# Kernel tuning notes

Measured on AMD Instinct MI355X. Metric: run time of the kernel, lower is better.

The kernel has to match this reference:

```python
import jax, jax.numpy as jnp
import numpy as np

B, S, D, H, DK, DV = 4, 2048, 1024, 16, 64, 64

def setup_inputs() -> dict:
    key = jax.random.key(0)
    ks = jax.random.split(key, 7)
    scale = 0.02
    queries = jax.random.normal(ks[0], (B, S, D), jnp.float32)
    keys_ = jax.random.normal(ks[1], (B, S, D), jnp.float32)
    values = jax.random.normal(ks[2], (B, S, D), jnp.float32)
    # causal mask: 1 where attendable, 0 where masked
    mask = jnp.tril(jnp.ones((S, S), jnp.int32))[None, None, :, :]
    W_Q = jax.random.normal(ks[3], (D, H * DK), jnp.float32) * scale
    W_K = jax.random.normal(ks[4], (D, H * DK), jnp.float32) * scale
    W_V = jax.random.normal(ks[5], (D, H * DV), jnp.float32) * scale
    W_O = jax.random.normal(ks[6], (H * DV, D), jnp.float32) * scale
    return {"queries": queries, "keys": keys_, "values": values, "mask": mask,
            "W_Q": W_Q, "W_K": W_K, "W_V": W_V, "W_O": W_O}

def reference(queries, keys, values, mask, W_Q, W_K, W_V, W_O):
    b, skv, _ = keys.shape
    sq = queries.shape[1]
    scaling = 1.0 / (DK ** 0.5)
    Q = (queries @ W_Q).reshape(b, sq, H, DK)   # [B,Sq,H,DK]
    K = (keys @ W_K).reshape(b, skv, H, DK)     # [B,Skv,H,DK]
    V = (values @ W_V).reshape(b, skv, H, DV)   # [B,Skv,H,DV]
    scores = jnp.einsum('bqhd,bkhd->bhqk', Q, K)
    scores = jnp.where(mask == 0, -jnp.inf, scores)
    probs = jax.nn.softmax(scores * scaling, axis=-1)
    attn = jnp.einsum('bhqk,bkhd->bqhd', probs, V).reshape(b, sq, H * DV)
    return attn @ W_O
```

## Files before the change

### kernel.cpp

```cpp
#include <hip/hip_runtime.h>
#include <hip/hip_bf16.h>


typedef __attribute__((ext_vector_type(8))) __bf16 bf16x8;
typedef __attribute__((ext_vector_type(8))) unsigned short ushort8v;
typedef __attribute__((ext_vector_type(4))) unsigned short ushort4v;
typedef __attribute__((ext_vector_type(4))) unsigned uint4v;
typedef __attribute__((ext_vector_type(2))) unsigned uint2v;
typedef __attribute__((ext_vector_type(4))) float float4v;

#define MFMA16(a, b, c) __builtin_amdgcn_mfma_f32_16x16x32_bf16((a), (b), (c), 0, 0, 0)
#define GLDS16(g, l)                                                     \
    __builtin_amdgcn_global_load_lds(                                    \
        (const __attribute__((address_space(1))) void*)(g),              \
        (__attribute__((address_space(3))) void*)(l), 16, 0, 0)

__device__ __forceinline__ unsigned short f2bf(float f) {
    union { float f; unsigned u; } v; v.f = f;
    unsigned r = v.u + 0x7fffu + ((v.u >> 16) & 1u);
    return (unsigned short)(r >> 16);
}
__device__ __forceinline__ unsigned pkbf(float a, float b) {
    union { float f; unsigned u; } x, y; x.f = a; y.f = b;
    return __builtin_amdgcn_perm(y.u + 0x8000u, x.u + 0x8000u, 0x07060302u);
}
__device__ __forceinline__ float exp2_fast(float x) {
#if __has_builtin(__builtin_amdgcn_exp2f)
    return __builtin_amdgcn_exp2f(x);
#else
    return __builtin_exp2f(x);
#endif
}

__global__ __launch_bounds__(256) void transpose_w4(
    const float* __restrict__ W0, const float* __restrict__ W1,
    const float* __restrict__ W2, const float* __restrict__ W3,
    unsigned short* __restrict__ T0, unsigned short* __restrict__ T1,
    unsigned short* __restrict__ T2, unsigned short* __restrict__ T3)
{
    __shared__ unsigned short T[64][72];
    const int z = blockIdx.z;
    const float* W = z == 0 ? W0 : z == 1 ? W1 : z == 2 ? W2 : W3;
    unsigned short* Wt = z == 0 ? T0 : z == 1 ? T1 : z == 2 ? T2 : T3;
    const float scale = (z == 1) ? 0.125f * 1.44269504088896f : 1.0f;
    const int t = threadIdx.x;
    const int n0 = blockIdx.x * 64, k0 = blockIdx.y * 64;
    for (int i = 0; i < 4; i++) {
        int idx = i * 256 + t, r = idx >> 4, c = (idx & 15) * 4;
        float4v v = *(const float4v*)&W[(size_t)(k0 + r) * 1024 + n0 + c];
        T[c + 0][r] = f2bf(v.x * scale); T[c + 1][r] = f2bf(v.y * scale);
        T[c + 2][r] = f2bf(v.z * scale); T[c + 3][r] = f2bf(v.w * scale);
    }
    __syncthreads();
    for (int i = 0; i < 4; i++) {
        int idx = i * 256 + t, r = idx >> 4, c = (idx & 15) * 4;
        ushort4v o; o.x = T[r][c]; o.y = T[r][c + 1]; o.z = T[r][c + 2]; o.w = T[r][c + 3];
        *(ushort4v*)&Wt[(size_t)(n0 + r) * 1024 + k0 + c] = o;
    }
}

__global__ __launch_bounds__(256) void qkv_gemm(
    const float* __restrict__ Aq, const float* __restrict__ Ak,
    const float* __restrict__ Av,
    const unsigned short* __restrict__ WQt, const unsigned short* __restrict__ WKt,
    const unsigned short* __restrict__ WVt,
    unsigned short* __restrict__ Qb, unsigned short* __restrict__ Kb,
    unsigned short* __restrict__ Vto)
{
    __shared__ __align__(16) unsigned short As[128 * 64];
    __shared__ __align__(16) unsigned short Bs[128 * 64];

    const int t = threadIdx.x;
    const int lane = t & 63, w = t >> 6;
    const int lanelo = lane & 15, quad = lane >> 4;
    const int wm = w >> 1, wn = w & 1;
    const int rsw = (lanelo & 7) << 3;

    const int d = blockIdx.x;
    const int xcd = d & 7;
    const int s = d >> 3;
    const int group = s >> 6;
    const int u = s & 63;
    const bool vsw = (group == 2);

    const float* act; const unsigned short* wt; unsigned short* out;
    if (group == 0)      { act = Aq; wt = WQt; out = Qb; }
    else if (group == 1) { act = Ak; wt = WKt; out = Kb; }
    else                 { act = Av; wt = WVt; out = Vto; }

    const int big = (((u >> 3) << 3) | xcd) * 128;
    const int sml = (u & 7) * 128;
    int m0, n0, ldc;
    if (!vsw) { m0 = big; n0 = sml; ldc = 1024; }
    else      { n0 = big; m0 = sml; ldc = 8192; }
    const int act0 = vsw ? n0 : m0;
    const int wt0  = vsw ? m0 : n0;
    unsigned short* actS = vsw ? Bs : As;
    unsigned short* wtS  = vsw ? As : Bs;

    float4v acc[4][4];
    for (int i = 0; i < 4; i++)
        for (int j = 0; j < 4; j++) acc[i][j] = (float4v)(0.f);

    for (int k0 = 0; k0 < 1024; k0 += 64) {
        for (int i = 0; i < 4; i++) {
            int idx = i * 256 + t, row = idx >> 3, ch = idx & 7;
            GLDS16(wt + (size_t)(wt0 + row) * 1024 + k0 + ((ch ^ (row & 7)) << 3),
                   &wtS[idx * 8]);
        }
        for (int i = 0; i < 4; i++) {
            int si = i * 256 + t, row = si >> 3, ch = si & 7;
            const float* ap = act + (size_t)(act0 + row) * 1024 + k0 + ch * 8;
            float4v x = *(const float4v*)ap;
            float4v y = *(const float4v*)(ap + 4);
            uint4v o4 = { pkbf(x.x, x.y), pkbf(x.z, x.w),
                          pkbf(y.x, y.y), pkbf(y.z, y.w) };
            *(uint4v*)&actS[row * 64 + ((ch ^ (row & 7)) << 3)] = o4;
        }
        __syncthreads();
        for (int ks = 0; ks < 2; ks++) {
            bf16x8 af[4], bfr[4];
            for (int mi = 0; mi < 4; mi++)
                af[mi] = *(const bf16x8*)
                    &As[(wm * 64 + mi * 16 + lanelo) * 64 + ((ks * 32 + quad * 8) ^ rsw)];
            for (int ni = 0; ni < 4; ni++)
                bfr[ni] = *(const bf16x8*)
                    &Bs[(wn * 64 + ni * 16 + lanelo) * 64 + ((ks * 32 + quad * 8) ^ rsw)];
            for (int mi = 0; mi < 4; mi++)
                for (int ni = 0; ni < 4; ni++)
                    acc[mi][ni] = MFMA16(af[mi], bfr[ni], acc[mi][ni]);
        }
        __syncthreads();
    }

    for (int mi = 0; mi < 4; mi++)
        for (int ni = 0; ni < 4; ni++) {
            int col = n0 + wn * 64 + ni * 16 + lanelo;
            for (int rr = 0; rr < 4; rr++) {
                int row = m0 + wm * 64 + mi * 16 + quad * 4 + rr;
                out[(size_t)row * ldc + col] = f2bf(acc[mi][ni][rr]);
            }
        }
}

__global__ __launch_bounds__(256) void gemm_bb(
    const unsigned short* __restrict__ A, const unsigned short* __restrict__ Bt,
    float* __restrict__ Cp, int M, int N, int K)
{
    __shared__ __align__(16) unsigned short As[128 * 64];
    __shared__ __align__(16) unsigned short Bs[128 * 64];

    const int t = threadIdx.x;
    const int lane = t & 63, w = t >> 6;
    const int lanelo = lane & 15, quad = lane >> 4;
    const int wm = w >> 1, wn = w & 1;
    const int rsw = (lanelo & 7) << 3;

    const int d = blockIdx.x;
    const int xcd = d & 7, s = d >> 3;
    const int m0 = ((((s >> 3) << 3) | xcd)) * 128;
    const int n0 = (s & 7) * 128;

    float4v acc[4][4];
    for (int i = 0; i < 4; i++)
        for (int j = 0; j < 4; j++) acc[i][j] = (float4v)(0.f);

    for (int k0 = 0; k0 < K; k0 += 64) {
        for (int i = 0; i < 4; i++) {
            int idx = i * 256 + t, row = idx >> 3, ch = idx & 7;
            GLDS16(A + (size_t)(m0 + row) * K + k0 + ((ch ^ (row & 7)) << 3),
                   &As[idx * 8]);
        }
        for (int i = 0; i < 4; i++) {
            int idx = i * 256 + t, row = idx >> 3, ch = idx & 7;
            GLDS16(Bt + (size_t)(n0 + row) * K + k0 + ((ch ^ (row & 7)) << 3),
                   &Bs[idx * 8]);
        }
        __syncthreads();
        for (int ks = 0; ks < 2; ks++) {
            bf16x8 af[4], bfr[4];
            for (int mi = 0; mi < 4; mi++)
                af[mi] = *(const bf16x8*)
                    &As[(wm * 64 + mi * 16 + lanelo) * 64 + ((ks * 32 + quad * 8) ^ rsw)];
            for (int ni = 0; ni < 4; ni++)
                bfr[ni] = *(const bf16x8*)
                    &Bs[(wn * 64 + ni * 16 + lanelo) * 64 + ((ks * 32 + quad * 8) ^ rsw)];
            for (int mi = 0; mi < 4; mi++)
                for (int ni = 0; ni < 4; ni++)
                    acc[mi][ni] = MFMA16(af[mi], bfr[ni], acc[mi][ni]);
        }
        __syncthreads();
    }

    for (int mi = 0; mi < 4; mi++)
        for (int ni = 0; ni < 4; ni++) {
            int col = n0 + wn * 64 + ni * 16 + lanelo;
            for (int r = 0; r < 4; r++) {
                int row = m0 + wm * 64 + mi * 16 + quad * 4 + r;
                Cp[(size_t)row * N + col] = acc[mi][ni][r];
            }
        }
}

__global__ __launch_bounds__(256, 4) void attn_k(
    const unsigned short* __restrict__ Qb, const unsigned short* __restrict__ Kb,
    const unsigned short* __restrict__ Vt, unsigned short* __restrict__ Ob)
{
    __shared__ __align__(16) unsigned short Ks[2][64 * 64];
    __shared__ __align__(16) unsigned short Vs[2][64 * 64];
    __shared__ __align__(16) unsigned short Ps[4][16 * 64];

    const int t = threadIdx.x;
    const int lane = t & 63, w = t >> 6;
    const int lanelo = lane & 15, quad = lane >> 4;
    const int bh = blockIdx.x;
    const int b = bh >> 4, h = bh & 15;

    unsigned short* pw = &Ps[w][0];
    const int rsw = (lanelo & 7) * 8;
    const int l7 = lanelo & 7;

    auto stage = [&](int buf, int kt) {
        for (int i = 0; i < 2; i++) {
            int idx = i * 256 + t, row = idx >> 3, ch = idx & 7;
            GLDS16(Kb + ((size_t)(b * 2048 + kt * 64 + row)) * 1024 + h * 64
                       + ((ch ^ (row & 7)) << 3),
                   &Ks[buf][idx * 8]);
        }
        for (int i = 0; i < 2; i++) {
            int idx = i * 256 + t, row = idx >> 3, ch = idx & 7;
            GLDS16(Vt + (size_t)(h * 64 + row) * 8192 + b * 2048 + kt * 64
                       + ((ch ^ (row & 7)) << 3),
                   &Vs[buf][idx * 8]);
        }
    };

    for (int half = 0; half < 2; half++) {
        const int qt = half ? blockIdx.y : 31 - blockIdx.y;
        const int qb = qt * 64;
        const int nkt = qt + 1;
        const int q = qb + w * 16 + lanelo;

        bf16x8 qf[2];
        {
            const unsigned short* qp = Qb + ((size_t)(b * 2048) + q) * 1024 + h * 64 + quad * 8;
            qf[0] = *(const bf16x8*)(qp);
            qf[1] = *(const bf16x8*)(qp + 32);
        }
        float4v o[4];
        for (int i = 0; i < 4; i++) o[i] = (float4v)(0.f);
        float m_ = -__builtin_inff(), l_ = 0.f;

        stage(0, 0);
        __syncthreads();

        int cur = 0;
        for (int kt = 0; kt < nkt; kt++) {
            if (kt + 1 < nkt) stage(cur ^ 1, kt + 1);

            const unsigned short* ks = &Ks[cur][0];
            const unsigned short* vs = &Vs[cur][0];

            float4v sc[4];
            for (int nt = 0; nt < 4; nt++) {
                sc[nt] = (float4v)(0.f);
                for (int c = 0; c < 2; c++) {
                    bf16x8 kf = *(const bf16x8*)
                        &ks[(nt * 16 + lanelo) * 64 + ((c * 32 + quad * 8) ^ rsw)];
                    sc[nt] = MFMA16(kf, qf[c], sc[nt]);
                }
            }
            if (kt == nkt - 1) {
                const int kb0 = qb + quad * 4;
                for (int nt = 0; nt < 4; nt++)
                    for (int r = 0; r < 4; r++)
                        if (kb0 + nt * 16 + r > q) sc[nt][r] = -__builtin_inff();
            }
            float mx = sc[0][0];
            for (int nt = 0; nt < 4; nt++)
                for (int r = 0; r < 4; r++) mx = fmaxf(mx, sc[nt][r]);
            mx = fmaxf(mx, __shfl_xor(mx, 16, 64));
            mx = fmaxf(mx, __shfl_xor(mx, 32, 64));
            if (!__all(mx <= m_ + 8.f)) {
                float mnew = fmaxf(m_, mx);
                float alpha = exp2_fast(m_ - mnew);
                l_ *= alpha;
                for (int vt = 0; vt < 4; vt++)
                    for (int r = 0; r < 4; r++) o[vt][r] *= alpha;
                m_ = mnew;
            }
            float rs = 0.f;
            for (int nt = 0; nt < 4; nt++)
                for (int r = 0; r < 4; r++) {
                    float e = exp2_fast(sc[nt][r] - m_);
                    sc[nt][r] = e; rs += e;
                }
            rs += __shfl_xor(rs, 16, 64);
            rs += __shfl_xor(rs, 32, 64);
            l_ += rs;

            for (int nt = 0; nt < 4; nt++) {
                uint2v pv;
                pv.x = pkbf(sc[nt][0], sc[nt][1]);
                pv.y = pkbf(sc[nt][2], sc[nt][3]);
                *(uint2v*)((char*)pw + lanelo * 128
                           + ((((nt << 1) | (quad >> 1)) ^ l7) << 4)
                           + ((quad & 1) << 3)) = pv;
            }
            asm volatile("s_waitcnt lgkmcnt(0)" ::: "memory");
            __builtin_amdgcn_sched_barrier(0);
            for (int c = 0; c < 2; c++) {
                bf16x8 pf = *(const bf16x8*)((const char*)pw + lanelo * 128
                                             + (((c * 4 + quad) ^ l7) << 4));
                for (int vt = 0; vt < 4; vt++) {
                    bf16x8 vf = *(const bf16x8*)
                        &vs[(vt * 16 + lanelo) * 64 + ((c * 32 + quad * 8) ^ rsw)];
                    o[vt] = MFMA16(vf, pf, o[vt]);
                }
            }
            __syncthreads();
            cur ^= 1;
        }

        float inv = 1.0f / l_;
        for (int vt = 0; vt < 4; vt++) {
            uint2v ov;
            ov.x = pkbf(o[vt][0] * inv, o[vt][1] * inv);
            ov.y = pkbf(o[vt][2] * inv, o[vt][3] * inv);
            *(uint2v*)((char*)pw + lanelo * 128
                       + ((((vt << 1) | (quad >> 1)) ^ l7) << 4)
                       + ((quad & 1) << 3)) = ov;
        }
        asm volatile("s_waitcnt lgkmcnt(0)" ::: "memory");
        __builtin_amdgcn_sched_barrier(0);
        for (int i = 0; i < 2; i++) {
            int qr = i * 8 + (lane >> 3);
            int ch = lane & 7;
            ushort8v ov = *(const ushort8v*)((const char*)pw + qr * 128
                                             + ((ch ^ (qr & 7)) << 4));
            *(ushort8v*)(Ob + ((size_t)(b * 2048) + qb + w * 16 + qr) * 1024
                         + h * 64 + ch * 8) = ov;
        }
    }
}

extern "C" void kernel_launch(void* const* d_in, const int* in_sizes, int n_in,
                              void* d_out, int out_size, void* d_ws, size_t ws_size,
                              hipStream_t stream) {
    const float* queries = (const float*)d_in[0];
    const float* keys    = (const float*)d_in[1];
    const float* values  = (const float*)d_in[2];
    const float* W_Q = (const float*)d_in[4];
    const float* W_K = (const float*)d_in[5];
    const float* W_V = (const float*)d_in[6];
    const float* W_O = (const float*)d_in[7];

    const size_t SZ = (size_t)4 * 2048 * 1024;
    const size_t WSZ = (size_t)1024 * 1024;
    unsigned short* Qb  = (unsigned short*)d_ws;
    unsigned short* Kb  = Qb + SZ;
    unsigned short* Vt  = Kb + SZ;
    unsigned short* Ab  = Vt + SZ;
    unsigned short* WQt = Ab + SZ;
    unsigned short* WKt = WQt + WSZ;
    unsigned short* WVt = WKt + WSZ;
    unsigned short* WOt = WVt + WSZ;

    dim3 blk(256);
    hipLaunchKernelGGL(transpose_w4, dim3(16, 16, 4), blk, 0, stream,
                       W_Q, W_K, W_V, W_O, WQt, WKt, WVt, WOt);

    hipLaunchKernelGGL(qkv_gemm, dim3(1536), blk, 0, stream,
                       queries, keys, values, WQt, WKt, WVt, Qb, Kb, Vt);

    hipLaunchKernelGGL(attn_k, dim3(64, 16), blk, 0, stream, Qb, Kb, Vt, Ab);

    hipLaunchKernelGGL(gemm_bb, dim3(512), blk, 0, stream,
                       Ab, WOt, (float*)d_out, 8192, 1024, 1024);
}
```

Before: 314.9 us.

## Double-buffer gemm_bb LDS tiles and use partial vmcnt waits in attention

The output-projection GEMM now double-buffers its A/B LDS tiles, issuing the next k-tile's global-to-LDS loads before computing on the current one and waiting only for the older batch with a partial vmcnt. The attention kernel replaces its full __syncthreads with partial vmcnt waits plus raw barriers, so prefetch loads of the next K/V tile can stay in flight during compute. This aims to overlap memory latency with MFMA work. The cost is doubled LDS in the GEMM, which may reduce occupancy. Correctness now depends on hand-counted vmcnt values and the hardcoded 16-iteration loop, which assumes K=1024.

```diff
diff --git a/kernel.cpp b/kernel.cpp
--- a/kernel.cpp
+++ b/kernel.cpp
@@ -147,8 +147,8 @@
     const unsigned short* __restrict__ A, const unsigned short* __restrict__ Bt,
     float* __restrict__ Cp, int M, int N, int K)
 {
-    __shared__ __align__(16) unsigned short As[128 * 64];
-    __shared__ __align__(16) unsigned short Bs[128 * 64];
+    __shared__ __align__(16) unsigned short As[2][128 * 64];
+    __shared__ __align__(16) unsigned short Bs[2][128 * 64];
 
     const int t = threadIdx.x;
     const int lane = t & 63, w = t >> 6;
@@ -161,35 +161,48 @@
     const int m0 = ((((s >> 3) << 3) | xcd)) * 128;
     const int n0 = (s & 7) * 128;
 
+    auto stage = [&](int buf, int k0) {
+        for (int i = 0; i < 4; i++) {
+            int idx = i * 256 + t, row = idx >> 3, ch = idx & 7;
+            GLDS16(A + (size_t)(m0 + row) * K + k0 + ((ch ^ (row & 7)) << 3),
+                   &As[buf][idx * 8]);
+        }
+        for (int i = 0; i < 4; i++) {
+            int idx = i * 256 + t, row = idx >> 3, ch = idx & 7;
+            GLDS16(Bt + (size_t)(n0 + row) * K + k0 + ((ch ^ (row & 7)) << 3),
+                   &Bs[buf][idx * 8]);
+        }
+    };
+
     float4v acc[4][4];
     for (int i = 0; i < 4; i++)
         for (int j = 0; j < 4; j++) acc[i][j] = (float4v)(0.f);
 
-    for (int k0 = 0; k0 < K; k0 += 64) {
-        for (int i = 0; i < 4; i++) {
-            int idx = i * 256 + t, row = idx >> 3, ch = idx & 7;
-            GLDS16(A + (size_t)(m0 + row) * K + k0 + ((ch ^ (row & 7)) << 3),
-                   &As[idx * 8]);
-        }
-        for (int i = 0; i < 4; i++) {
-            int idx = i * 256 + t, row = idx >> 3, ch = idx & 7;
-            GLDS16(Bt + (size_t)(n0 + row) * K + k0 + ((ch ^ (row & 7)) << 3),
-                   &Bs[idx * 8]);
-        }
-        __syncthreads();
+    stage(0, 0);
+    for (int tt = 0; tt < 16; ++tt) {
+        const int cur = tt & 1;
+        if (tt + 1 < 16) {
+            stage(cur ^ 1, (tt + 1) * 64);
+            asm volatile("s_waitcnt vmcnt(8)" ::: "memory");
+        } else {
+            asm volatile("s_waitcnt vmcnt(0)" ::: "memory");
+        }
+        __builtin_amdgcn_s_barrier();
+        __builtin_amdgcn_sched_barrier(0);
         for (int ks = 0; ks < 2; ks++) {
             bf16x8 af[4], bfr[4];
             for (int mi = 0; mi < 4; mi++)
                 af[mi] = *(const bf16x8*)
-                    &As[(wm * 64 + mi * 16 + lanelo) * 64 + ((ks * 32 + quad * 8) ^ rsw)];
+                    &As[cur][(wm * 64 + mi * 16 + lanelo) * 64 + ((ks * 32 + quad * 8) ^ rsw)];
             for (int ni = 0; ni < 4; ni++)
                 bfr[ni] = *(const bf16x8*)
-                    &Bs[(wn * 64 + ni * 16 + lanelo) * 64 + ((ks * 32 + quad * 8) ^ rsw)];
+                    &Bs[cur][(wn * 64 + ni * 16 + lanelo) * 64 + ((ks * 32 + quad * 8) ^ rsw)];
             for (int mi = 0; mi < 4; mi++)
                 for (int ni = 0; ni < 4; ni++)
                     acc[mi][ni] = MFMA16(af[mi], bfr[ni], acc[mi][ni]);
         }
-        __syncthreads();
+        __builtin_amdgcn_sched_barrier(0);
+        __builtin_amdgcn_s_barrier();
     }
 
     for (int mi = 0; mi < 4; mi++)
@@ -252,11 +265,17 @@
         float m_ = -__builtin_inff(), l_ = 0.f;
 
         stage(0, 0);
-        __syncthreads();
 
         int cur = 0;
         for (int kt = 0; kt < nkt; kt++) {
-            if (kt + 1 < nkt) stage(cur ^ 1, kt + 1);
+            if (kt + 1 < nkt) {
+                stage(cur ^ 1, kt + 1);
+                asm volatile("s_waitcnt vmcnt(4)" ::: "memory");
+            } else {
+                asm volatile("s_waitcnt vmcnt(0)" ::: "memory");
+            }
+            __builtin_amdgcn_s_barrier();
+            __builtin_amdgcn_sched_barrier(0);
 
             const unsigned short* ks = &Ks[cur][0];
             const unsigned short* vs = &Vs[cur][0];
@@ -318,7 +337,8 @@
                     o[vt] = MFMA16(vf, pf, o[vt]);
                 }
             }
-            __syncthreads();
+            __builtin_amdgcn_sched_barrier(0);
+            __builtin_amdgcn_s_barrier();
             cur ^= 1;
         }
 
```

Result: no change. 312.7 us (median of 2 runs) (-0.7%).

## Split-K output GEMM with atomics and finer-grained waits in attention loop

Applied to the files above, without the earlier changes.

The output-projection GEMM is split in two along K, launching 1024 blocks instead of 512 for better occupancy. Partial results are accumulated into a zeroed output with float atomicAdd, which adds a memset and atomic traffic. Separately, the attention kernel replaces __syncthreads with explicit vmcnt waits and raw barriers, so the prefetch of the next K/V tile can stay in flight while the current tile is consumed. The correctness of vmcnt(4) relies on stage() issuing exactly four loads per thread, and the atomics make the summation order nondeterministic.

```diff
diff --git a/kernel.cpp b/kernel.cpp
--- a/kernel.cpp
+++ b/kernel.cpp
@@ -143,7 +143,7 @@
         }
 }
 
-__global__ __launch_bounds__(256) void gemm_bb(
+__global__ __launch_bounds__(256) void gemm_bb_sk(
     const unsigned short* __restrict__ A, const unsigned short* __restrict__ Bt,
     float* __restrict__ Cp, int M, int N, int K)
 {
@@ -158,14 +158,18 @@
 
     const int d = blockIdx.x;
     const int xcd = d & 7, s = d >> 3;
-    const int m0 = ((((s >> 3) << 3) | xcd)) * 128;
-    const int n0 = (s & 7) * 128;
+    const int ksl = s >> 6;
+    const int u = s & 63;
+    const int m0 = (((u >> 3) << 3) | xcd) * 128;
+    const int n0 = (u & 7) * 128;
+    const int kbeg = ksl * 512;
 
     float4v acc[4][4];
     for (int i = 0; i < 4; i++)
         for (int j = 0; j < 4; j++) acc[i][j] = (float4v)(0.f);
 
-    for (int k0 = 0; k0 < K; k0 += 64) {
+    for (int kk = 0; kk < 512; kk += 64) {
+        const int k0 = kbeg + kk;
         for (int i = 0; i < 4; i++) {
             int idx = i * 256 + t, row = idx >> 3, ch = idx & 7;
             GLDS16(A + (size_t)(m0 + row) * K + k0 + ((ch ^ (row & 7)) << 3),
@@ -197,7 +201,7 @@
             int col = n0 + wn * 64 + ni * 16 + lanelo;
             for (int r = 0; r < 4; r++) {
                 int row = m0 + wm * 64 + mi * 16 + quad * 4 + r;
-                Cp[(size_t)row * N + col] = acc[mi][ni][r];
+                atomicAdd(&Cp[(size_t)row * N + col], acc[mi][ni][r]);
             }
         }
 }
@@ -252,11 +256,17 @@
         float m_ = -__builtin_inff(), l_ = 0.f;
 
         stage(0, 0);
-        __syncthreads();
 
         int cur = 0;
         for (int kt = 0; kt < nkt; kt++) {
-            if (kt + 1 < nkt) stage(cur ^ 1, kt + 1);
+            if (kt + 1 < nkt) {
+                stage(cur ^ 1, kt + 1);
+                asm volatile("s_waitcnt vmcnt(4)" ::: "memory");
+            } else {
+                asm volatile("s_waitcnt vmcnt(0)" ::: "memory");
+            }
+            __builtin_amdgcn_s_barrier();
+            __builtin_amdgcn_sched_barrier(0);
 
             const unsigned short* ks = &Ks[cur][0];
             const unsigned short* vs = &Vs[cur][0];
@@ -318,7 +328,8 @@
                     o[vt] = MFMA16(vf, pf, o[vt]);
                 }
             }
-            __syncthreads();
+            __builtin_amdgcn_sched_barrier(0);
+            __builtin_amdgcn_s_barrier();
             cur ^= 1;
         }
 
@@ -375,6 +386,7 @@
 
     hipLaunchKernelGGL(attn_k, dim3(64, 16), blk, 0, stream, Qb, Kb, Vt, Ab);
 
-    hipLaunchKernelGGL(gemm_bb, dim3(512), blk, 0, stream,
+    hipMemsetAsync(d_out, 0, (size_t)8192 * 1024 * sizeof(float), stream);
+    hipLaunchKernelGGL(gemm_bb_sk, dim3(1024), blk, 0, stream,
                        Ab, WOt, (float*)d_out, 8192, 1024, 1024);
 }
```

After: 360.6 us. 1.15x slower.
